# Kernel optimization log

Hardware: AMD Instinct MI355X
Metric: run time of the kernel (lower is better)

## Reference

```python
import jax, jax.numpy as jnp
import numpy as np

HEAD = 12
HEAD_DIM = 64  # dim // head = 768 // 12


def setup_inputs() -> dict:
    key = jax.random.key(0)
    k1, k2, k3 = jax.random.split(key, 3)
    B, N, D = 4, 2048, 768
    scale = 1.0 / np.sqrt(D)
    return {
        "x": jax.random.normal(k1, (B, N, D), dtype=jnp.float32),
        "w_qkv": jax.random.normal(k2, (D, 3 * D), dtype=jnp.float32) * scale,
        "w_proj": jax.random.normal(k3, (D, D), dtype=jnp.float32) * scale,
        "b_proj": jnp.zeros((D,), dtype=jnp.float32),
    }


def reference(x, w_qkv, w_proj, b_proj):
    B, N, D = x.shape
    qkv = x @ w_qkv  # [B, N, 3D]
    q, k, v = jnp.split(qkv, 3, axis=-1)
    # [B, H, N, k]
    def heads(t):
        return t.reshape(B, N, HEAD, HEAD_DIM).transpose(0, 2, 1, 3)
    q, k, v = heads(q), heads(k), heads(v)
    attn = jnp.einsum("bhnd,bhmd->bhnm", q, k) / jnp.sqrt(jnp.float32(HEAD_DIM))
    attn_prob = jax.nn.softmax(attn, axis=-1)  # dropout p=0.0 -> identity
    out = jnp.einsum("bhnm,bhmd->bhnd", attn_prob, v)
    out = out.transpose(0, 2, 1, 3).reshape(B, N, D)
    return out @ w_proj + b_proj
```

## Files before the change

### kernel.cpp

```cpp
#include <hip/hip_runtime.h>

typedef unsigned short u16;
typedef unsigned int u32;
typedef u16 u16x4 __attribute__((ext_vector_type(4)));
typedef u16 u16x8 __attribute__((ext_vector_type(8)));
typedef u32 u32x2 __attribute__((ext_vector_type(2)));
typedef u32 u32x4 __attribute__((ext_vector_type(4)));
typedef __bf16 bf16x8 __attribute__((ext_vector_type(8)));
typedef float f32x4 __attribute__((ext_vector_type(4)));
typedef float f32x16 __attribute__((ext_vector_type(16)));

#define MFMA16 __builtin_amdgcn_mfma_f32_16x16x32_bf16
#define MFMA32 __builtin_amdgcn_mfma_f32_32x32x16_bf16

__device__ __forceinline__ u16 f2bf(float f) {
  return __builtin_bit_cast(u16, (__bf16)f);
}

__device__ __forceinline__ u32 pk2bf(float a, float b) {
  return (u32)__builtin_bit_cast(u16, (__bf16)a) |
         ((u32)__builtin_bit_cast(u16, (__bf16)b) << 16);
}

__device__ __forceinline__ u32x2 swap32(u32 a, u32 b, int hi) {
#if __has_builtin(__builtin_amdgcn_permlane32_swap)
  (void)hi;
  return __builtin_amdgcn_permlane32_swap(a, b, false, false);
#else
  u32 sa = (u32)__shfl_xor((int)a, 32), sb = (u32)__shfl_xor((int)b, 32);
  u32x2 r;
  r[0] = hi ? sb : a;
  r[1] = hi ? b : sa;
  return r;
#endif
}

__device__ __forceinline__ void gload_lds16(const void* g, void* l) {
  __builtin_amdgcn_global_load_lds(
      (const __attribute__((address_space(1))) u32*)g,
      (__attribute__((address_space(3))) u32*)l, 16, 0, 0);
}

__global__ void cvt_f32_bf16_kernel(const float* __restrict__ in,
                                    u16* __restrict__ out, int n4) {
  int i = blockIdx.x * blockDim.x + threadIdx.x;
  if (i >= n4) return;
  float4 v = reinterpret_cast<const float4*>(in)[i];
  u16x4 o;
  o[0] = f2bf(v.x); o[1] = f2bf(v.y); o[2] = f2bf(v.z); o[3] = f2bf(v.w);
  reinterpret_cast<u16x4*>(out)[i] = o;
}

__global__ void transpose_cvt_kernel(const float* __restrict__ w,
                                     u16* __restrict__ wt, int K, int N) {
  __shared__ float t[32][33];
  int bk = blockIdx.x * 32, bn = blockIdx.y * 32;
  int x = threadIdx.x, y = threadIdx.y;
#pragma unroll
  for (int j = 0; j < 32; j += 8)
    t[y + j][x] = w[(size_t)(bk + y + j) * N + bn + x];
  __syncthreads();
#pragma unroll
  for (int j = 0; j < 32; j += 8)
    wt[(size_t)(bn + y + j) * K + bk + x] = f2bf(t[x][y + j]);
}

#define QSCALE 0.18033688011112042f

template <int NTOT, int EPI, int NT>
__global__ __launch_bounds__(256)
void gemm_bf16_kernel(const u16* __restrict__ A, const u16* __restrict__ BT,
                      u16* __restrict__ qo, u16* __restrict__ ko,
                      u16* __restrict__ vt, float* __restrict__ outF,
                      const float* __restrict__ bias) {
  __shared__ u16 sh[16384];
  u16* As = sh;
  u16* Bs = sh + 8192;
  const int tid = threadIdx.x;
  const int l = tid & 63, w = tid >> 6;
  const int lr = l & 15, lg = l >> 4;
  const int swz = (blockIdx.x & 7) * (8 * NT) + (blockIdx.x >> 3);
  const int mtile = swz / NT;
  const int ntile = swz % NT;
  const int mbase = mtile * 128, nbase = ntile * 128;
  const int wr = (w >> 1) * 64, wc = (w & 1) * 64;

  f32x4 acc[4][4] = {};

  for (int k0 = 0; k0 < 768; k0 += 64) {
#pragma unroll
    for (int i = 0; i < 4; ++i) {
      const int c = w * 64 + i * 256 + l;
      const int row = c >> 3, c16 = c & 7;
      const int sc = c16 ^ (row & 7);
      gload_lds16(A + (size_t)(mbase + row) * 768 + k0 + sc * 8,
                  &As[(size_t)(w * 64 + i * 256) * 8]);
      gload_lds16(BT + (size_t)(nbase + row) * 768 + k0 + sc * 8,
                  &Bs[(size_t)(w * 64 + i * 256) * 8]);
    }
    __syncthreads();
#pragma unroll
    for (int ks = 0; ks < 2; ++ks) {
      bf16x8 af[4], bfr[4];
#pragma unroll
      for (int m = 0; m < 4; ++m) {
        const int row = wr + m * 16 + lr;
        const int byte = (row * 128 + ks * 64 + lg * 16) ^ ((row & 7) << 4);
        af[m] = *reinterpret_cast<const bf16x8*>((const char*)As + byte);
      }
#pragma unroll
      for (int n = 0; n < 4; ++n) {
        const int row = wc + n * 16 + lr;
        const int byte = (row * 128 + ks * 64 + lg * 16) ^ ((row & 7) << 4);
        bfr[n] = *reinterpret_cast<const bf16x8*>((const char*)Bs + byte);
      }
#pragma unroll
      for (int m = 0; m < 4; ++m)
#pragma unroll
        for (int n = 0; n < 4; ++n)
          acc[m][n] = MFMA16(af[m], bfr[n], acc[m][n], 0, 0, 0);
    }
    __syncthreads();
  }

  if (EPI == 0 && ntile >= 12) {
    u16* vts = sh;
#pragma unroll
    for (int m = 0; m < 4; ++m)
#pragma unroll
      for (int n = 0; n < 4; ++n)
#pragma unroll
        for (int r = 0; r < 4; ++r) {
          const int col = wc + n * 16 + lr;
          const int row = wr + m * 16 + lg * 4 + r;
          const int byte = col * 256 + ((row * 2) ^ ((col & 7) << 4));
          *reinterpret_cast<u16*>((char*)vts + byte) = f2bf(acc[m][n][r]);
        }
    __syncthreads();
    const int b2 = mbase >> 11, nn0 = mbase & 2047;
#pragma unroll
    for (int i = 0; i < 8; ++i) {
      const int idx = i * 256 + tid;
      const int col = idx >> 4, u = idx & 15;
      u16x8 vv = *reinterpret_cast<u16x8*>(
          (char*)vts + (col * 256 + ((u * 16) ^ ((col & 7) << 4))));
      const int cg = nbase - 1536 + col;
      const int hh = cg >> 6, dd = cg & 63;
      *reinterpret_cast<u16x8*>(
          vt + (((size_t)(b2 * 12 + hh)) * 64 + dd) * 2048 + nn0 + u * 8) = vv;
    }
    return;
  }

#pragma unroll
  for (int m = 0; m < 4; ++m) {
#pragma unroll
    for (int n = 0; n < 4; ++n) {
#pragma unroll
      for (int r = 0; r < 4; ++r) {
        const int row = mbase + wr + m * 16 + lg * 4 + r;
        const int col = nbase + wc + n * 16 + lr;
        float val = acc[m][n][r];
        if (EPI == 0) {
          const int w2 = col / 768;
          const int c2 = col - w2 * 768;
          const int hh = c2 >> 6, dd = c2 & 63;
          const int b2 = row >> 11, nn = row & 2047;
          u16* dst = (w2 == 0) ? qo : ko;
          if (w2 == 0) val *= QSCALE;
          dst[(((size_t)(b2 * 12 + hh)) * 2048 + nn) * 64 + dd] = f2bf(val);
        } else {
          outF[(size_t)row * NTOT + col] = val + bias[col];
        }
      }
    }
  }
}

__global__ __launch_bounds__(256)
void flash_attn32_kernel(const u16* __restrict__ qb, const u16* __restrict__ kb,
                         const u16* __restrict__ vtb, u16* __restrict__ ao) {
  __shared__ u16 sh[32768];
  const int tid = threadIdx.x, w = tid >> 6, l = tid & 63;
  const int q5 = l & 31, hi = l >> 5;
  const int swz = (blockIdx.x & 7) * 96 + (blockIdx.x >> 3);
  const int bh = swz >> 4, qt = swz & 15;
  const int b = bh / 12, h = bh % 12;
  const int qrow0 = qt * 128 + w * 32;
  const u16* Q = qb + ((size_t)bh * 2048 + qrow0) * 64;
  const u16* K = kb + (size_t)bh * 2048 * 64;
  const u16* Vg = vtb + (size_t)bh * 64 * 2048;

  bf16x8 qf[4];
#pragma unroll
  for (int dk = 0; dk < 4; ++dk)
    qf[dk] = *reinterpret_cast<const bf16x8*>(Q + (size_t)q5 * 64 + dk * 16 + hi * 8);

  f32x16 ot0 = {}, ot1 = {};
  float l_ = 0.f;

  auto stage2 = [&](u16* base, int kt0) {
#pragma unroll
    for (int s = 0; s < 2; ++s) {
      u16* sb = base + s * 8192;
      const int kt = kt0 + s * 64;
#pragma unroll
      for (int i = 0; i < 2; ++i) {
        const int c = w * 64 + i * 256 + l;
        const int L = c >> 4, C = (c & 15) ^ (L & 15);
        const int row = L + ((C >> 3) << 5);
        gload_lds16(K + (size_t)(kt + row) * 64 + (C & 7) * 8,
                    sb + (size_t)(w * 64 + i * 256) * 8);
      }
#pragma unroll
      for (int i = 0; i < 2; ++i) {
        const int c = w * 64 + i * 256 + l;
        const int L = c >> 4, C = (c & 15) ^ (L & 15);
        const int d = L + ((C >> 3) << 5);
        gload_lds16(Vg + (size_t)d * 2048 + kt + (C & 7) * 8,
                    sb + 4096 + (size_t)(w * 64 + i * 256) * 8);
      }
    }
  };

  stage2(sh, 0);
  int cur = 0;
  const int q15 = q5 & 15;

  for (int win = 0; win < 16; ++win) {
    u16* tb = sh + cur * 16384;
    __builtin_amdgcn_sched_barrier(0);
    __builtin_amdgcn_s_barrier();
    __builtin_amdgcn_sched_barrier(0);
    if (win + 1 < 16) {
      stage2(sh + (cur ^ 1) * 16384, (win + 1) * 128);
      asm volatile("s_waitcnt vmcnt(8)" ::: "memory");
    } else {
      asm volatile("s_waitcnt vmcnt(0)" ::: "memory");
    }
    __builtin_amdgcn_sched_barrier(0);
    __builtin_amdgcn_s_barrier();
    __builtin_amdgcn_sched_barrier(0);

    for (int s = 0; s < 2; ++s) {
      const char* ksb = (const char*)(tb + s * 8192);
      const char* vsb = (const char*)(tb + s * 8192 + 4096);

      f32x16 st0 = {}, st1 = {};
      __builtin_amdgcn_s_setprio(1);
#pragma unroll
      for (int dk = 0; dk < 4; ++dk) {
        const int C = dk * 2 + hi;
        bf16x8 kf0 = *reinterpret_cast<const bf16x8*>(
            ksb + q5 * 256 + ((C ^ q15) << 4));
        bf16x8 kf1 = *reinterpret_cast<const bf16x8*>(
            ksb + q5 * 256 + (((C + 8) ^ q15) << 4));
        st0 = MFMA32(kf0, qf[dk], st0, 0, 0, 0);
        st1 = MFMA32(kf1, qf[dk], st1, 0, 0, 0);
      }
      __builtin_amdgcn_s_setprio(0);

      float ls = 0.f;
#pragma unroll
      for (int r = 0; r < 16; ++r) {
        st0[r] = __builtin_amdgcn_exp2f(st0[r]); ls += st0[r];
      }
#pragma unroll
      for (int r = 0; r < 16; ++r) {
        st1[r] = __builtin_amdgcn_exp2f(st1[r]); ls += st1[r];
      }
      l_ += ls + __shfl_xor(ls, 32);

      __builtin_amdgcn_s_setprio(1);
#pragma unroll
      for (int kvs = 0; kvs < 4; ++kvs) {
        const f32x16& stx = (kvs < 2) ? st0 : st1;
        const int rb = (kvs & 1) * 8;
        const u32 A0 = pk2bf(stx[rb + 0], stx[rb + 1]);
        const u32 A1 = pk2bf(stx[rb + 2], stx[rb + 3]);
        const u32 A2 = pk2bf(stx[rb + 4], stx[rb + 5]);
        const u32 A3 = pk2bf(stx[rb + 6], stx[rb + 7]);
        const u32x2 p02 = swap32(A0, A2, hi);
        const u32x2 p13 = swap32(A1, A3, hi);
        u32x4 wv;
        wv[0] = p02[0]; wv[1] = p13[0]; wv[2] = p02[1]; wv[3] = p13[1];
        const bf16x8 pf = __builtin_bit_cast(bf16x8, wv);
        const int Cv = kvs * 2 + hi;
        bf16x8 vf0 = *reinterpret_cast<const bf16x8*>(
            vsb + q5 * 256 + ((Cv ^ q15) << 4));
        bf16x8 vf1 = *reinterpret_cast<const bf16x8*>(
            vsb + q5 * 256 + (((Cv + 8) ^ q15) << 4));
        ot0 = MFMA32(vf0, pf, ot0, 0, 0, 0);
        ot1 = MFMA32(vf1, pf, ot1, 0, 0, 0);
      }
      __builtin_amdgcn_s_setprio(0);
    }
    cur ^= 1;
  }

  u16* ob = sh + w * 2048;
  const float inv = 1.0f / l_;
  const int swo = (q5 & 7) << 4;
#pragma unroll
  for (int g = 0; g < 4; ++g) {
    u16x4 pk0, pk1;
#pragma unroll
    for (int r = 0; r < 4; ++r) {
      pk0[r] = f2bf(ot0[g * 4 + r] * inv);
      pk1[r] = f2bf(ot1[g * 4 + r] * inv);
    }
    const int d0 = hi * 4 + g * 8;
    *reinterpret_cast<u16x4*>((char*)ob + ((q5 * 128 + d0 * 2) ^ swo)) = pk0;
    *reinterpret_cast<u16x4*>((char*)ob + ((q5 * 128 + (d0 + 32) * 2) ^ swo)) = pk1;
  }
  __syncthreads();
#pragma unroll
  for (int i = 0; i < 4; ++i) {
    const int idx = i * 64 + l;
    const int qr = idx >> 3, cc = idx & 7;
    u16x8 vv = *reinterpret_cast<u16x8*>(
        (char*)ob + ((qr * 128 + cc * 16) ^ ((qr & 7) << 4)));
    *reinterpret_cast<u16x8*>(
        ao + ((size_t)(b * 2048 + qrow0 + qr)) * 768 + h * 64 + cc * 8) = vv;
  }
}

extern "C" void kernel_launch(void* const* d_in, const int* in_sizes, int n_in,
                              void* d_out, int out_size, void* d_ws,
                              size_t ws_size, hipStream_t stream) {
  const float* x = (const float*)d_in[0];
  const float* w_qkv = (const float*)d_in[1];
  const float* w_proj = (const float*)d_in[2];
  const float* b_proj = (const float*)d_in[3];
  float* out = (float*)d_out;

  char* ws = (char*)d_ws;
  size_t off = 0;
  auto alloc = [&](size_t bytes) {
    char* p = ws + off;
    off += (bytes + 255) & ~(size_t)255;
    return p;
  };
  u16* xb = (u16*)alloc(8192ull * 768 * 2);
  u16* wqkvT = (u16*)alloc(2304ull * 768 * 2);
  u16* wprojT = (u16*)alloc(768ull * 768 * 2);
  u16* qbuf = (u16*)alloc(48ull * 2048 * 64 * 2);
  u16* kbuf = (u16*)alloc(48ull * 2048 * 64 * 2);
  u16* vtb = (u16*)alloc(48ull * 64 * 2048 * 2);
  u16* aob = (u16*)alloc(8192ull * 768 * 2);
  (void)ws_size; (void)n_in; (void)in_sizes; (void)out_size;

  cvt_f32_bf16_kernel<<<(8192 * 768 / 4) / 256, 256, 0, stream>>>(
      x, xb, 8192 * 768 / 4);
  transpose_cvt_kernel<<<dim3(768 / 32, 2304 / 32), dim3(32, 8), 0, stream>>>(
      w_qkv, wqkvT, 768, 2304);
  transpose_cvt_kernel<<<dim3(768 / 32, 768 / 32), dim3(32, 8), 0, stream>>>(
      w_proj, wprojT, 768, 768);

  gemm_bf16_kernel<2304, 0, 18><<<64 * 18, 256, 0, stream>>>(
      xb, wqkvT, qbuf, kbuf, vtb, nullptr, nullptr);

  flash_attn32_kernel<<<768, 256, 0, stream>>>(qbuf, kbuf, vtb, aob);

  gemm_bf16_kernel<768, 1, 6><<<64 * 6, 256, 0, stream>>>(
      aob, wprojT, nullptr, nullptr, nullptr, out, b_proj);
}
```

Measured before the change: 157.3 us.

## Merge conversion prepasses into one launch and batch both KV sub-tiles in attention

The three preprocessing launches (x to bf16 conversion plus two weight transpose-converts) become a single kernel that uses block-index ranges to pick its job, saving two launches and their gaps. In the flash attention loop, the two 64-key sub-tiles per window are now processed together. All four QK^T MFMA chains are issued back to back and all exps computed before either PV pass, giving more independent MFMA work to hide latency. The cost is more live accumulator registers (four f32x16 score tiles), which may lower occupancy or cause spills.

```diff
diff --git a/kernel.cpp b/kernel.cpp
--- a/kernel.cpp
+++ b/kernel.cpp
@@ -41,28 +41,35 @@
       (__attribute__((address_space(3))) u32*)l, 16, 0, 0);
 }
 
-__global__ void cvt_f32_bf16_kernel(const float* __restrict__ in,
-                                    u16* __restrict__ out, int n4) {
-  int i = blockIdx.x * blockDim.x + threadIdx.x;
-  if (i >= n4) return;
-  float4 v = reinterpret_cast<const float4*>(in)[i];
-  u16x4 o;
-  o[0] = f2bf(v.x); o[1] = f2bf(v.y); o[2] = f2bf(v.z); o[3] = f2bf(v.w);
-  reinterpret_cast<u16x4*>(out)[i] = o;
-}
-
-__global__ void transpose_cvt_kernel(const float* __restrict__ w,
-                                     u16* __restrict__ wt, int K, int N) {
+__global__ __launch_bounds__(256)
+void prepass_kernel(const float* __restrict__ x, u16* __restrict__ xb,
+                    const float* __restrict__ wq, u16* __restrict__ wqT,
+                    const float* __restrict__ wp, u16* __restrict__ wpT) {
   __shared__ float t[32][33];
-  int bk = blockIdx.x * 32, bn = blockIdx.y * 32;
-  int x = threadIdx.x, y = threadIdx.y;
+  const int bid = blockIdx.x, tid = threadIdx.x;
+  if (bid < 6144) {
+    const int i = bid * 256 + tid;
+    float4 v = reinterpret_cast<const float4*>(x)[i];
+    u16x4 o;
+    o[0] = f2bf(v.x); o[1] = f2bf(v.y); o[2] = f2bf(v.z); o[3] = f2bf(v.w);
+    reinterpret_cast<u16x4*>(xb)[i] = o;
+    return;
+  }
+  const float* w;
+  u16* wt;
+  int N, b2;
+  if (bid < 7872) { b2 = bid - 6144; w = wq; wt = wqT; N = 2304; }
+  else            { b2 = bid - 7872; w = wp; wt = wpT; N = 768; }
+  const int K = 768;
+  const int bk = (b2 % 24) * 32, bn = (b2 / 24) * 32;
+  const int xx = tid & 31, yy = tid >> 5;
 #pragma unroll
   for (int j = 0; j < 32; j += 8)
-    t[y + j][x] = w[(size_t)(bk + y + j) * N + bn + x];
+    t[yy + j][xx] = w[(size_t)(bk + yy + j) * N + bn + xx];
   __syncthreads();
 #pragma unroll
   for (int j = 0; j < 32; j += 8)
-    wt[(size_t)(bn + y + j) * K + bk + x] = f2bf(t[x][y + j]);
+    wt[(size_t)(bn + yy + j) * K + bk + xx] = f2bf(t[xx][yy + j]);
 }
 
 #define QSCALE 0.18033688011112042f
@@ -242,59 +249,94 @@
     __builtin_amdgcn_s_barrier();
     __builtin_amdgcn_sched_barrier(0);
 
-    for (int s = 0; s < 2; ++s) {
-      const char* ksb = (const char*)(tb + s * 8192);
-      const char* vsb = (const char*)(tb + s * 8192 + 4096);
-
-      f32x16 st0 = {}, st1 = {};
-      __builtin_amdgcn_s_setprio(1);
-#pragma unroll
-      for (int dk = 0; dk < 4; ++dk) {
-        const int C = dk * 2 + hi;
-        bf16x8 kf0 = *reinterpret_cast<const bf16x8*>(
-            ksb + q5 * 256 + ((C ^ q15) << 4));
-        bf16x8 kf1 = *reinterpret_cast<const bf16x8*>(
-            ksb + q5 * 256 + (((C + 8) ^ q15) << 4));
-        st0 = MFMA32(kf0, qf[dk], st0, 0, 0, 0);
-        st1 = MFMA32(kf1, qf[dk], st1, 0, 0, 0);
-      }
-      __builtin_amdgcn_s_setprio(0);
-
-      float ls = 0.f;
-#pragma unroll
-      for (int r = 0; r < 16; ++r) {
-        st0[r] = __builtin_amdgcn_exp2f(st0[r]); ls += st0[r];
-      }
-#pragma unroll
-      for (int r = 0; r < 16; ++r) {
-        st1[r] = __builtin_amdgcn_exp2f(st1[r]); ls += st1[r];
-      }
-      l_ += ls + __shfl_xor(ls, 32);
-
-      __builtin_amdgcn_s_setprio(1);
-#pragma unroll
-      for (int kvs = 0; kvs < 4; ++kvs) {
-        const f32x16& stx = (kvs < 2) ? st0 : st1;
-        const int rb = (kvs & 1) * 8;
-        const u32 A0 = pk2bf(stx[rb + 0], stx[rb + 1]);
-        const u32 A1 = pk2bf(stx[rb + 2], stx[rb + 3]);
-        const u32 A2 = pk2bf(stx[rb + 4], stx[rb + 5]);
-        const u32 A3 = pk2bf(stx[rb + 6], stx[rb + 7]);
-        const u32x2 p02 = swap32(A0, A2, hi);
-        const u32x2 p13 = swap32(A1, A3, hi);
-        u32x4 wv;
-        wv[0] = p02[0]; wv[1] = p13[0]; wv[2] = p02[1]; wv[3] = p13[1];
-        const bf16x8 pf = __builtin_bit_cast(bf16x8, wv);
-        const int Cv = kvs * 2 + hi;
-        bf16x8 vf0 = *reinterpret_cast<const bf16x8*>(
-            vsb + q5 * 256 + ((Cv ^ q15) << 4));
-        bf16x8 vf1 = *reinterpret_cast<const bf16x8*>(
-            vsb + q5 * 256 + (((Cv + 8) ^ q15) << 4));
-        ot0 = MFMA32(vf0, pf, ot0, 0, 0, 0);
-        ot1 = MFMA32(vf1, pf, ot1, 0, 0, 0);
-      }
-      __builtin_amdgcn_s_setprio(0);
-    }
+    const char* ksbA = (const char*)tb;
+    const char* vsbA = (const char*)(tb + 4096);
+    const char* ksbB = (const char*)(tb + 8192);
+    const char* vsbB = (const char*)(tb + 12288);
+
+    f32x16 sA0 = {}, sA1 = {}, sB0 = {}, sB1 = {};
+    __builtin_amdgcn_s_setprio(1);
+#pragma unroll
+    for (int dk = 0; dk < 4; ++dk) {
+      const int C = dk * 2 + hi;
+      const int o0 = (C ^ q15) << 4, o1 = (((C + 8) ^ q15)) << 4;
+      bf16x8 ka0 = *reinterpret_cast<const bf16x8*>(ksbA + q5 * 256 + o0);
+      bf16x8 ka1 = *reinterpret_cast<const bf16x8*>(ksbA + q5 * 256 + o1);
+      bf16x8 kb0 = *reinterpret_cast<const bf16x8*>(ksbB + q5 * 256 + o0);
+      bf16x8 kb1 = *reinterpret_cast<const bf16x8*>(ksbB + q5 * 256 + o1);
+      sA0 = MFMA32(ka0, qf[dk], sA0, 0, 0, 0);
+      sA1 = MFMA32(ka1, qf[dk], sA1, 0, 0, 0);
+      sB0 = MFMA32(kb0, qf[dk], sB0, 0, 0, 0);
+      sB1 = MFMA32(kb1, qf[dk], sB1, 0, 0, 0);
+    }
+    __builtin_amdgcn_s_setprio(0);
+
+    float lsA = 0.f, lsB = 0.f;
+#pragma unroll
+    for (int r = 0; r < 16; ++r) {
+      sA0[r] = __builtin_amdgcn_exp2f(sA0[r]); lsA += sA0[r];
+    }
+#pragma unroll
+    for (int r = 0; r < 16; ++r) {
+      sA1[r] = __builtin_amdgcn_exp2f(sA1[r]); lsA += sA1[r];
+    }
+#pragma unroll
+    for (int r = 0; r < 16; ++r) {
+      sB0[r] = __builtin_amdgcn_exp2f(sB0[r]); lsB += sB0[r];
+    }
+#pragma unroll
+    for (int r = 0; r < 16; ++r) {
+      sB1[r] = __builtin_amdgcn_exp2f(sB1[r]); lsB += sB1[r];
+    }
+    l_ += lsA + __shfl_xor(lsA, 32);
+
+    __builtin_amdgcn_s_setprio(1);
+#pragma unroll
+    for (int kvs = 0; kvs < 4; ++kvs) {
+      const f32x16& stx = (kvs < 2) ? sA0 : sA1;
+      const int rb = (kvs & 1) * 8;
+      const u32 A0 = pk2bf(stx[rb + 0], stx[rb + 1]);
+      const u32 A1 = pk2bf(stx[rb + 2], stx[rb + 3]);
+      const u32 A2 = pk2bf(stx[rb + 4], stx[rb + 5]);
+      const u32 A3 = pk2bf(stx[rb + 6], stx[rb + 7]);
+      const u32x2 p02 = swap32(A0, A2, hi);
+      const u32x2 p13 = swap32(A1, A3, hi);
+      u32x4 wv;
+      wv[0] = p02[0]; wv[1] = p13[0]; wv[2] = p02[1]; wv[3] = p13[1];
+      const bf16x8 pf = __builtin_bit_cast(bf16x8, wv);
+      const int Cv = kvs * 2 + hi;
+      bf16x8 vf0 = *reinterpret_cast<const bf16x8*>(
+          vsbA + q5 * 256 + ((Cv ^ q15) << 4));
+      bf16x8 vf1 = *reinterpret_cast<const bf16x8*>(
+          vsbA + q5 * 256 + (((Cv + 8) ^ q15) << 4));
+      ot0 = MFMA32(vf0, pf, ot0, 0, 0, 0);
+      ot1 = MFMA32(vf1, pf, ot1, 0, 0, 0);
+    }
+    __builtin_amdgcn_s_setprio(0);
+    l_ += lsB + __shfl_xor(lsB, 32);
+    __builtin_amdgcn_s_setprio(1);
+#pragma unroll
+    for (int kvs = 0; kvs < 4; ++kvs) {
+      const f32x16& stx = (kvs < 2) ? sB0 : sB1;
+      const int rb = (kvs & 1) * 8;
+      const u32 A0 = pk2bf(stx[rb + 0], stx[rb + 1]);
+      const u32 A1 = pk2bf(stx[rb + 2], stx[rb + 3]);
+      const u32 A2 = pk2bf(stx[rb + 4], stx[rb + 5]);
+      const u32 A3 = pk2bf(stx[rb + 6], stx[rb + 7]);
+      const u32x2 p02 = swap32(A0, A2, hi);
+      const u32x2 p13 = swap32(A1, A3, hi);
+      u32x4 wv;
+      wv[0] = p02[0]; wv[1] = p13[0]; wv[2] = p02[1]; wv[3] = p13[1];
+      const bf16x8 pf = __builtin_bit_cast(bf16x8, wv);
+      const int Cv = kvs * 2 + hi;
+      bf16x8 vf0 = *reinterpret_cast<const bf16x8*>(
+          vsbB + q5 * 256 + ((Cv ^ q15) << 4));
+      bf16x8 vf1 = *reinterpret_cast<const bf16x8*>(
+          vsbB + q5 * 256 + (((Cv + 8) ^ q15) << 4));
+      ot0 = MFMA32(vf0, pf, ot0, 0, 0, 0);
+      ot1 = MFMA32(vf1, pf, ot1, 0, 0, 0);
+    }
+    __builtin_amdgcn_s_setprio(0);
     cur ^= 1;
   }
 
@@ -350,12 +392,7 @@
   u16* aob = (u16*)alloc(8192ull * 768 * 2);
   (void)ws_size; (void)n_in; (void)in_sizes; (void)out_size;
 
-  cvt_f32_bf16_kernel<<<(8192 * 768 / 4) / 256, 256, 0, stream>>>(
-      x, xb, 8192 * 768 / 4);
-  transpose_cvt_kernel<<<dim3(768 / 32, 2304 / 32), dim3(32, 8), 0, stream>>>(
-      w_qkv, wqkvT, 768, 2304);
-  transpose_cvt_kernel<<<dim3(768 / 32, 768 / 32), dim3(32, 8), 0, stream>>>(
-      w_proj, wprojT, 768, 768);
+  prepass_kernel<<<8448, 256, 0, stream>>>(x, xb, w_qkv, wqkvT, w_proj, wprojT);
 
   gemm_bf16_kernel<2304, 0, 18><<<64 * 18, 256, 0, stream>>>(
       xb, wqkvT, qbuf, kbuf, vtb, nullptr, nullptr);
```

Result: faster. 151.7 us (-3.5%).

## Load K/V fragments directly from global in attention; merge prepass kernels

Applied to the files above, without the earlier changes.

The attention kernel no longer stages K and V tiles through double-buffered LDS with barriers. Each lane now loads its MFMA fragments straight from global memory into registers, and the shared buffer shrinks to what the output epilogue needs. Separately, the three conversion/transpose launches are merged into one prepass kernel to cut launch overhead. The trade-off is that the four waves of a block now load the same K/V data separately, which relies on L1/L2 reuse, and global latency is exposed without an explicit prefetch pipeline.

```diff
diff --git a/kernel.cpp b/kernel.cpp
--- a/kernel.cpp
+++ b/kernel.cpp
@@ -41,28 +41,35 @@
       (__attribute__((address_space(3))) u32*)l, 16, 0, 0);
 }
 
-__global__ void cvt_f32_bf16_kernel(const float* __restrict__ in,
-                                    u16* __restrict__ out, int n4) {
-  int i = blockIdx.x * blockDim.x + threadIdx.x;
-  if (i >= n4) return;
-  float4 v = reinterpret_cast<const float4*>(in)[i];
-  u16x4 o;
-  o[0] = f2bf(v.x); o[1] = f2bf(v.y); o[2] = f2bf(v.z); o[3] = f2bf(v.w);
-  reinterpret_cast<u16x4*>(out)[i] = o;
-}
-
-__global__ void transpose_cvt_kernel(const float* __restrict__ w,
-                                     u16* __restrict__ wt, int K, int N) {
+__global__ __launch_bounds__(256)
+void prepass_kernel(const float* __restrict__ x, u16* __restrict__ xb,
+                    const float* __restrict__ wq, u16* __restrict__ wqT,
+                    const float* __restrict__ wp, u16* __restrict__ wpT) {
   __shared__ float t[32][33];
-  int bk = blockIdx.x * 32, bn = blockIdx.y * 32;
-  int x = threadIdx.x, y = threadIdx.y;
+  const int bid = blockIdx.x, tid = threadIdx.x;
+  if (bid < 6144) {
+    const int i = bid * 256 + tid;
+    float4 v = reinterpret_cast<const float4*>(x)[i];
+    u16x4 o;
+    o[0] = f2bf(v.x); o[1] = f2bf(v.y); o[2] = f2bf(v.z); o[3] = f2bf(v.w);
+    reinterpret_cast<u16x4*>(xb)[i] = o;
+    return;
+  }
+  const float* w;
+  u16* wt;
+  int N, b2;
+  if (bid < 7872) { b2 = bid - 6144; w = wq; wt = wqT; N = 2304; }
+  else            { b2 = bid - 7872; w = wp; wt = wpT; N = 768; }
+  const int K = 768;
+  const int bk = (b2 % 24) * 32, bn = (b2 / 24) * 32;
+  const int xx = tid & 31, yy = tid >> 5;
 #pragma unroll
   for (int j = 0; j < 32; j += 8)
-    t[y + j][x] = w[(size_t)(bk + y + j) * N + bn + x];
+    t[yy + j][xx] = w[(size_t)(bk + yy + j) * N + bn + xx];
   __syncthreads();
 #pragma unroll
   for (int j = 0; j < 32; j += 8)
-    wt[(size_t)(bn + y + j) * K + bk + x] = f2bf(t[x][y + j]);
+    wt[(size_t)(bn + yy + j) * K + bk + xx] = f2bf(t[xx][yy + j]);
 }
 
 #define QSCALE 0.18033688011112042f
@@ -180,7 +187,7 @@
 __global__ __launch_bounds__(256)
 void flash_attn32_kernel(const u16* __restrict__ qb, const u16* __restrict__ kb,
                          const u16* __restrict__ vtb, u16* __restrict__ ao) {
-  __shared__ u16 sh[32768];
+  __shared__ u16 sh[8192];
   const int tid = threadIdx.x, w = tid >> 6, l = tid & 63;
   const int q5 = l & 31, hi = l >> 5;
   const int swz = (blockIdx.x & 7) * 96 + (blockIdx.x >> 3);
@@ -196,106 +203,68 @@
   for (int dk = 0; dk < 4; ++dk)
     qf[dk] = *reinterpret_cast<const bf16x8*>(Q + (size_t)q5 * 64 + dk * 16 + hi * 8);
 
+  const u16* K0 = K + (size_t)q5 * 64 + hi * 8;
+  const u16* K1 = K + (size_t)(q5 + 32) * 64 + hi * 8;
+  const u16* V0 = Vg + (size_t)q5 * 2048 + hi * 8;
+  const u16* V1 = Vg + (size_t)(q5 + 32) * 2048 + hi * 8;
+
   f32x16 ot0 = {}, ot1 = {};
   float l_ = 0.f;
 
-  auto stage2 = [&](u16* base, int kt0) {
-#pragma unroll
-    for (int s = 0; s < 2; ++s) {
-      u16* sb = base + s * 8192;
-      const int kt = kt0 + s * 64;
-#pragma unroll
-      for (int i = 0; i < 2; ++i) {
-        const int c = w * 64 + i * 256 + l;
-        const int L = c >> 4, C = (c & 15) ^ (L & 15);
-        const int row = L + ((C >> 3) << 5);
-        gload_lds16(K + (size_t)(kt + row) * 64 + (C & 7) * 8,
-                    sb + (size_t)(w * 64 + i * 256) * 8);
-      }
-#pragma unroll
-      for (int i = 0; i < 2; ++i) {
-        const int c = w * 64 + i * 256 + l;
-        const int L = c >> 4, C = (c & 15) ^ (L & 15);
-        const int d = L + ((C >> 3) << 5);
-        gload_lds16(Vg + (size_t)d * 2048 + kt + (C & 7) * 8,
-                    sb + 4096 + (size_t)(w * 64 + i * 256) * 8);
-      }
-    }
-  };
-
-  stage2(sh, 0);
-  int cur = 0;
-  const int q15 = q5 & 15;
-
-  for (int win = 0; win < 16; ++win) {
-    u16* tb = sh + cur * 16384;
-    __builtin_amdgcn_sched_barrier(0);
-    __builtin_amdgcn_s_barrier();
-    __builtin_amdgcn_sched_barrier(0);
-    if (win + 1 < 16) {
-      stage2(sh + (cur ^ 1) * 16384, (win + 1) * 128);
-      asm volatile("s_waitcnt vmcnt(8)" ::: "memory");
-    } else {
-      asm volatile("s_waitcnt vmcnt(0)" ::: "memory");
-    }
-    __builtin_amdgcn_sched_barrier(0);
-    __builtin_amdgcn_s_barrier();
-    __builtin_amdgcn_sched_barrier(0);
-
-    for (int s = 0; s < 2; ++s) {
-      const char* ksb = (const char*)(tb + s * 8192);
-      const char* vsb = (const char*)(tb + s * 8192 + 4096);
-
-      f32x16 st0 = {}, st1 = {};
-      __builtin_amdgcn_s_setprio(1);
-#pragma unroll
-      for (int dk = 0; dk < 4; ++dk) {
-        const int C = dk * 2 + hi;
-        bf16x8 kf0 = *reinterpret_cast<const bf16x8*>(
-            ksb + q5 * 256 + ((C ^ q15) << 4));
-        bf16x8 kf1 = *reinterpret_cast<const bf16x8*>(
-            ksb + q5 * 256 + (((C + 8) ^ q15) << 4));
-        st0 = MFMA32(kf0, qf[dk], st0, 0, 0, 0);
-        st1 = MFMA32(kf1, qf[dk], st1, 0, 0, 0);
-      }
-      __builtin_amdgcn_s_setprio(0);
-
-      float ls = 0.f;
-#pragma unroll
-      for (int r = 0; r < 16; ++r) {
-        st0[r] = __builtin_amdgcn_exp2f(st0[r]); ls += st0[r];
-      }
-#pragma unroll
-      for (int r = 0; r < 16; ++r) {
-        st1[r] = __builtin_amdgcn_exp2f(st1[r]); ls += st1[r];
-      }
-      l_ += ls + __shfl_xor(ls, 32);
-
-      __builtin_amdgcn_s_setprio(1);
-#pragma unroll
-      for (int kvs = 0; kvs < 4; ++kvs) {
-        const f32x16& stx = (kvs < 2) ? st0 : st1;
-        const int rb = (kvs & 1) * 8;
-        const u32 A0 = pk2bf(stx[rb + 0], stx[rb + 1]);
-        const u32 A1 = pk2bf(stx[rb + 2], stx[rb + 3]);
-        const u32 A2 = pk2bf(stx[rb + 4], stx[rb + 5]);
-        const u32 A3 = pk2bf(stx[rb + 6], stx[rb + 7]);
-        const u32x2 p02 = swap32(A0, A2, hi);
-        const u32x2 p13 = swap32(A1, A3, hi);
-        u32x4 wv;
-        wv[0] = p02[0]; wv[1] = p13[0]; wv[2] = p02[1]; wv[3] = p13[1];
-        const bf16x8 pf = __builtin_bit_cast(bf16x8, wv);
-        const int Cv = kvs * 2 + hi;
-        bf16x8 vf0 = *reinterpret_cast<const bf16x8*>(
-            vsb + q5 * 256 + ((Cv ^ q15) << 4));
-        bf16x8 vf1 = *reinterpret_cast<const bf16x8*>(
-            vsb + q5 * 256 + (((Cv + 8) ^ q15) << 4));
-        ot0 = MFMA32(vf0, pf, ot0, 0, 0, 0);
-        ot1 = MFMA32(vf1, pf, ot1, 0, 0, 0);
-      }
-      __builtin_amdgcn_s_setprio(0);
-    }
-    cur ^= 1;
+#pragma unroll 2
+  for (int t = 0; t < 32; ++t) {
+    const int kt = t * 64;
+
+    bf16x8 kf0[4], kf1[4], vf0[4], vf1[4];
+#pragma unroll
+    for (int dk = 0; dk < 4; ++dk) {
+      kf0[dk] = *reinterpret_cast<const bf16x8*>(K0 + (size_t)kt * 64 + dk * 16);
+      kf1[dk] = *reinterpret_cast<const bf16x8*>(K1 + (size_t)kt * 64 + dk * 16);
+    }
+#pragma unroll
+    for (int kvs = 0; kvs < 4; ++kvs) {
+      vf0[kvs] = *reinterpret_cast<const bf16x8*>(V0 + kt + kvs * 16);
+      vf1[kvs] = *reinterpret_cast<const bf16x8*>(V1 + kt + kvs * 16);
+    }
+
+    f32x16 st0 = {}, st1 = {};
+    __builtin_amdgcn_s_setprio(1);
+#pragma unroll
+    for (int dk = 0; dk < 4; ++dk) {
+      st0 = MFMA32(kf0[dk], qf[dk], st0, 0, 0, 0);
+      st1 = MFMA32(kf1[dk], qf[dk], st1, 0, 0, 0);
+    }
+    __builtin_amdgcn_s_setprio(0);
+
+    float ls = 0.f;
+#pragma unroll
+    for (int r = 0; r < 16; ++r) {
+      st0[r] = __builtin_amdgcn_exp2f(st0[r]); ls += st0[r];
+    }
+#pragma unroll
+    for (int r = 0; r < 16; ++r) {
+      st1[r] = __builtin_amdgcn_exp2f(st1[r]); ls += st1[r];
+    }
+    l_ += ls + __shfl_xor(ls, 32);
+
+    __builtin_amdgcn_s_setprio(1);
+#pragma unroll
+    for (int kvs = 0; kvs < 4; ++kvs) {
+      const f32x16& stx = (kvs < 2) ? st0 : st1;
+      const int rb = (kvs & 1) * 8;
+      const u32 A0 = pk2bf(stx[rb + 0], stx[rb + 1]);
+      const u32 A1 = pk2bf(stx[rb + 2], stx[rb + 3]);
+      const u32 A2 = pk2bf(stx[rb + 4], stx[rb + 5]);
+      const u32 A3 = pk2bf(stx[rb + 6], stx[rb + 7]);
+      const u32x2 p02 = swap32(A0, A2, hi);
+      const u32x2 p13 = swap32(A1, A3, hi);
+      u32x4 wv;
+      wv[0] = p02[0]; wv[1] = p13[0]; wv[2] = p02[1]; wv[3] = p13[1];
+      const bf16x8 pf = __builtin_bit_cast(bf16x8, wv);
+      ot0 = MFMA32(vf0[kvs], pf, ot0, 0, 0, 0);
+      ot1 = MFMA32(vf1[kvs], pf, ot1, 0, 0, 0);
+    }
+    __builtin_amdgcn_s_setprio(0);
   }
 
   u16* ob = sh + w * 2048;
@@ -350,12 +319,7 @@
   u16* aob = (u16*)alloc(8192ull * 768 * 2);
   (void)ws_size; (void)n_in; (void)in_sizes; (void)out_size;
 
-  cvt_f32_bf16_kernel<<<(8192 * 768 / 4) / 256, 256, 0, stream>>>(
-      x, xb, 8192 * 768 / 4);
-  transpose_cvt_kernel<<<dim3(768 / 32, 2304 / 32), dim3(32, 8), 0, stream>>>(
-      w_qkv, wqkvT, 768, 2304);
-  transpose_cvt_kernel<<<dim3(768 / 32, 768 / 32), dim3(32, 8), 0, stream>>>(
-      w_proj, wprojT, 768, 768);
+  prepass_kernel<<<8448, 256, 0, stream>>>(x, xb, w_qkv, wqkvT, w_proj, wprojT);
 
   gemm_bf16_kernel<2304, 0, 18><<<64 * 18, 256, 0, stream>>>(
       xb, wqkvT, qbuf, kbuf, vtb, nullptr, nullptr);
```

After: 250.3 us. 1.59x slower.
